# Kernel optimization log

Measured on AMD Instinct MI355X. Metric: run time of the kernel, lower is better.

The kernel has to match this reference:

```python
import jax, jax.numpy as jnp
import numpy as np

N_NODES = 100000
N_EDGES = 1600000
D = 128
N_LAYERS = 3
N_GRAPHS = 128


def setup_inputs() -> dict:
    key = jax.random.key(0)
    ks = jax.random.split(key, 8)
    x = jax.random.normal(ks[0], (N_NODES, D), dtype=jnp.float32)
    # stacked GIN-MLP params (all layers are D->D since hidden_dim == in_dim)
    scale = 1.0 / np.sqrt(D)
    W1 = jax.random.normal(ks[1], (N_LAYERS, D, D), dtype=jnp.float32) * scale
    b1 = jax.random.normal(ks[2], (N_LAYERS, D), dtype=jnp.float32) * 0.01
    W2 = jax.random.normal(ks[3], (N_LAYERS, D, D), dtype=jnp.float32) * scale
    b2 = jax.random.normal(ks[4], (N_LAYERS, D), dtype=jnp.float32) * 0.01
    edge_index = jax.random.randint(ks[5], (2, N_EDGES), 0, N_NODES, dtype=jnp.int64)
    batch = jnp.sort(jax.random.randint(ks[6], (N_NODES,), 0, N_GRAPHS, dtype=jnp.int64))
    return {"x": x, "W1": W1, "b1": b1, "W2": W2, "b2": b2,
            "edge_index": edge_index, "batch": batch}


def reference(x, W1, b1, W2, b2, edge_index, batch):
    src = edge_index[0]
    dst = edge_index[1]
    n = x.shape[0]
    eps = jnp.float32(0.0)  # GIN eps (PyG default, not trained)
    for i in range(N_LAYERS):
        # gather neighbor features along edges, scatter-add to destination nodes
        agg = jax.ops.segment_sum(x[src], dst, num_segments=n)  # [N, D]
        h = (1.0 + eps) * x + agg
        h = jax.nn.relu(h @ W1[i] + b1[i])
        x = h @ W2[i] + b2[i]
    # sum-pool readout per graph
    h_G = jax.ops.segment_sum(x, batch, num_segments=N_GRAPHS)  # [G, D]
    return h_G
```

## Files before the change

kernel.cpp:

```cpp
#include <hip/hip_runtime.h>
#include <hip/hip_bf16.h>
#include <stdint.h>

#define N_NODES 100000
#define N_EDGES 1600000
#define DIM 128
#define N_GRAPHS 128
#define LDA 136

#define NBKT 392
#define BCAP 6144
#define BP   5632

#define NBIN_BLK 391
#define CVT_BLK 3125

typedef unsigned int uint32;
typedef unsigned short ushort16;

typedef __bf16 bf16x8 __attribute__((ext_vector_type(8)));
typedef float fx4 __attribute__((ext_vector_type(4)));

__device__ __forceinline__ float bfLo(uint32 u){ return __builtin_bit_cast(float, (uint32)(u << 16)); }
__device__ __forceinline__ float bfHi(uint32 u){ return __builtin_bit_cast(float, (uint32)(u & 0xFFFF0000u)); }
__device__ __forceinline__ ushort16 f2bf(float f){
  uint32 u = __builtin_bit_cast(uint32, f);
  u = u + 0x7FFFu + ((u >> 16) & 1u);
  return (ushort16)(u >> 16);
}
__device__ __forceinline__ uint32 pack2(float a, float b){
  return (uint32)f2bf(a) | ((uint32)f2bf(b) << 16);
}

__global__ __launch_bounds__(512) void k_prep(const float* __restrict__ x,
                                              const float* __restrict__ W1, const float* __restrict__ W2,
                                              const int* __restrict__ ei,
                                              ushort16* __restrict__ P, ushort16* __restrict__ Q,
                                              ushort16* __restrict__ Wf,
                                              int* __restrict__ bucketCursor,
                                              int* __restrict__ temp){
  __shared__ int hist[NBKT];
  __shared__ int base[NBKT];
  __shared__ int gbase[NBKT];
  __shared__ int scanbuf[512];
  __shared__ int sVal[4096];
  __shared__ unsigned short sBkt[4096];

  int bb = blockIdx.x;
  int t  = threadIdx.x;

  if (bb < NBIN_BLK){
    int e0 = bb * 4096;
    for (int i = t; i < NBKT; i += 512) hist[i] = 0;
    __syncthreads();

    int   myv[8];
    short myb[8];
    short myr[8];
    #pragma unroll
    for (int it = 0; it < 8; ++it){
      int e = e0 + it*512 + t;
      int v = 0; short b = -1; short r = 0;
      if (e < N_EDGES){
        int s = ei[e];
        int d = ei[N_EDGES + e];
        b = (short)(d >> 8);
        v = s | ((d & 255) << 17);
        r = (short)atomicAdd(&hist[b], 1);
      }
      myv[it] = v; myb[it] = b; myr[it] = r;
    }
    __syncthreads();

    scanbuf[t] = (t < NBKT) ? hist[t] : 0;
    __syncthreads();
    for (int off = 1; off < 512; off <<= 1){
      int x2 = 0;
      if (t >= off) x2 = scanbuf[t - off];
      __syncthreads();
      scanbuf[t] += x2;
      __syncthreads();
    }
    if (t < NBKT){
      base[t]  = scanbuf[t] - hist[t];
      gbase[t] = atomicAdd(&bucketCursor[t], hist[t]);
    }
    __syncthreads();

    #pragma unroll
    for (int it = 0; it < 8; ++it){
      if (myb[it] >= 0){
        int p = base[myb[it]] + myr[it];
        sVal[p] = myv[it];
        sBkt[p] = (unsigned short)myb[it];
      }
    }
    __syncthreads();

    int cnt = scanbuf[NBKT - 1];
    for (int p = t; p < cnt; p += 512){
      int b = sBkt[p];
      int g = gbase[b] + (p - base[b]);
      if (g < BCAP) temp[b*BCAP + g] = sVal[p];
    }
    return;
  }

  if (bb < NBIN_BLK + CVT_BLK){
    int idx = ((bb - NBIN_BLK)*512 + t) * 8;
    float4 v0 = *(const float4*)(x + idx);
    float4 v1 = *(const float4*)(x + idx + 4);
    uint4 o;
    o.x = pack2(v0.x, v0.y); o.y = pack2(v0.z, v0.w);
    o.z = pack2(v1.x, v1.y); o.w = pack2(v1.z, v1.w);
    *(uint4*)(P + idx) = o;
    return;
  }

  if (bb == NBIN_BLK + CVT_BLK){
    uint4 z = {0u,0u,0u,0u};
    if (t < 16)                *(uint4*)(P + (size_t)N_NODES*128 + t*8)      = z;
    else if (t < 32)           *(uint4*)(Q + (size_t)N_NODES*128 + (t-16)*8) = z;
    return;
  }

  int tid = (bb - (NBIN_BLK + CVT_BLK + 1))*512 + t;
  int layer = tid >> 12;
  int rem   = tid & 4095;
  int mat   = rem >> 11;
  int nt    = (rem >> 8) & 7;
  int kt    = (rem >> 6) & 3;
  int lane  = rem & 63;
  int kg = lane >> 4, m = lane & 15;
  int n  = nt*16 + m;
  int kb = kt*32 + kg*8;
  const float* src = (mat ? W2 : W1) + layer*16384;
  uint4 o;
  o.x = pack2(src[(kb+0)*128 + n], src[(kb+1)*128 + n]);
  o.y = pack2(src[(kb+2)*128 + n], src[(kb+3)*128 + n]);
  o.z = pack2(src[(kb+4)*128 + n], src[(kb+5)*128 + n]);
  o.w = pack2(src[(kb+6)*128 + n], src[(kb+7)*128 + n]);
  *(uint4*)(Wf + ((((size_t)(layer*2+mat)*8 + nt)*4 + kt)*64 + lane)*8) = o;
}

__global__ __launch_bounds__(512) void k_binB(const int* __restrict__ temp,
                                              const int* __restrict__ bucketCursor,
                                              int* __restrict__ rowptr,
                                              int* __restrict__ rowlen,
                                              int* __restrict__ colx){
  __shared__ int counts[256];
  __shared__ int sc[256];
  __shared__ int cur[256];
  __shared__ int stage[BCAP];
  __shared__ int sorted[BCAP];
  int b = blockIdx.x, t = threadIdx.x;
  int cnt = min(bucketCursor[b], BCAP);
  int gb  = b * BP;
  const int* src = temp + b*BCAP;

  if (t < 256) counts[t] = 0;
  __syncthreads();
  for (int p = t; p < cnt; p += 512){
    int v = src[p];
    stage[p] = v;
    atomicAdd(&counts[v >> 17], 1);
  }
  __syncthreads();

  int len = 0, plen = 0;
  if (t < 256){
    len  = counts[t];
    plen = (len + 3) & ~3;
    sc[t] = plen;
  }
  __syncthreads();
  for (int off = 1; off < 256; off <<= 1){
    int x = 0;
    if (t < 256 && t >= off) x = sc[t - off];
    __syncthreads();
    if (t < 256) sc[t] += x;
    __syncthreads();
  }
  int excl = 0;
  if (t < 256){
    excl = sc[t] - plen;
    cur[t] = excl;
    int node = b*256 + t;
    if (node < N_NODES){ rowptr[node] = gb + excl; rowlen[node] = plen; }
  }
  __syncthreads();

  for (int p = t; p < cnt; p += 512){
    int v = stage[p];
    int d = v >> 17;
    int pos = atomicAdd(&cur[d], 1);
    sorted[pos] = v & 0x1FFFF;
  }
  __syncthreads();

  if (t < 256){
    for (int k = len; k < plen; ++k) sorted[excl + k] = N_NODES;
  }
  __syncthreads();

  int total = min(sc[255], BP);
  for (int p = t; p < total; p += 512) colx[gb + p] = sorted[p];
}

template<bool LAST>
__global__ __launch_bounds__(256, 8) void k_gin(const ushort16* __restrict__ xb, ushort16* __restrict__ hb,
                                                const ushort16* __restrict__ Wt1, const float* __restrict__ b1,
                                                const ushort16* __restrict__ Wt2, const float* __restrict__ b2,
                                                const int* __restrict__ rowptr, const int* __restrict__ rowlen,
                                                const int* __restrict__ colx,
                                                const int* __restrict__ batch, float* __restrict__ outp){
  __shared__ __attribute__((aligned(16))) ushort16 sA[32 * LDA];
  __shared__ int sOff[32];
  __shared__ int sLen[32];
  __shared__ int sBat[32];

  int t = threadIdx.x;
  int row0 = blockIdx.x * 32;

  if (t < 32){
    int gg = row0 + t;
    sOff[t] = rowptr[gg];
    sLen[t] = rowlen[gg];
    if (LAST) sBat[t] = batch[gg];
  }
  __syncthreads();

  int wave = t >> 6, lane = t & 63;
  int g = lane >> 4, o = lane & 15;
  const uint32* xw = (const uint32*)xb;

  for (int ni = 0; ni < 8; ++ni){
    int ln  = wave*8 + ni;
    int j   = __builtin_amdgcn_readfirstlane(sOff[ln]);
    int end = j + __builtin_amdgcn_readfirstlane(sLen[ln]);

    float f0=0.f,f1=0.f,f2=0.f,f3=0.f,f4=0.f,f5=0.f,f6=0.f,f7=0.f;

    while (j + 8 <= end){
      int4 c0 = *(const int4*)(colx + j);
      int4 c1 = *(const int4*)(colx + j + 4);
      int r0ab = (g & 1) ? c0.y : c0.x;
      int r0cd = (g & 1) ? c0.w : c0.z;
      int r0   = (g & 2) ? r0cd : r0ab;
      int r1ab = (g & 1) ? c1.y : c1.x;
      int r1cd = (g & 1) ? c1.w : c1.z;
      int r1   = (g & 2) ? r1cd : r1ab;
      uint4 u0 = *(const uint4*)(xw + (size_t)r0*64 + o*4);
      uint4 u1 = *(const uint4*)(xw + (size_t)r1*64 + o*4);
      f0 += bfLo(u0.x); f1 += bfHi(u0.x); f2 += bfLo(u0.y); f3 += bfHi(u0.y);
      f4 += bfLo(u0.z); f5 += bfHi(u0.z); f6 += bfLo(u0.w); f7 += bfHi(u0.w);
      f0 += bfLo(u1.x); f1 += bfHi(u1.x); f2 += bfLo(u1.y); f3 += bfHi(u1.y);
      f4 += bfLo(u1.z); f5 += bfHi(u1.z); f6 += bfLo(u1.w); f7 += bfHi(u1.w);
      j += 8;
    }
    if (j < end){
      int4 c0 = *(const int4*)(colx + j);
      int rab = (g & 1) ? c0.y : c0.x;
      int rcd = (g & 1) ? c0.w : c0.z;
      int r0  = (g & 2) ? rcd : rab;
      uint4 u0 = *(const uint4*)(xw + (size_t)r0*64 + o*4);
      f0 += bfLo(u0.x); f1 += bfHi(u0.x); f2 += bfLo(u0.y); f3 += bfHi(u0.y);
      f4 += bfLo(u0.z); f5 += bfHi(u0.z); f6 += bfLo(u0.w); f7 += bfHi(u0.w);
    }

    f0 += __shfl_xor(f0, 16, 64); f1 += __shfl_xor(f1, 16, 64);
    f2 += __shfl_xor(f2, 16, 64); f3 += __shfl_xor(f3, 16, 64);
    f4 += __shfl_xor(f4, 16, 64); f5 += __shfl_xor(f5, 16, 64);
    f6 += __shfl_xor(f6, 16, 64); f7 += __shfl_xor(f7, 16, 64);
    f0 += __shfl_xor(f0, 32, 64); f1 += __shfl_xor(f1, 32, 64);
    f2 += __shfl_xor(f2, 32, 64); f3 += __shfl_xor(f3, 32, 64);
    f4 += __shfl_xor(f4, 32, 64); f5 += __shfl_xor(f5, 32, 64);
    f6 += __shfl_xor(f6, 32, 64); f7 += __shfl_xor(f7, 32, 64);

    if (g == 0){
      int gn = row0 + ln;
      uint4 xv = *(const uint4*)(xw + (size_t)gn*64 + o*4);
      uint4 r;
      r.x = pack2(f0 + bfLo(xv.x), f1 + bfHi(xv.x));
      r.y = pack2(f2 + bfLo(xv.y), f3 + bfHi(xv.y));
      r.z = pack2(f4 + bfLo(xv.z), f5 + bfHi(xv.z));
      r.w = pack2(f6 + bfLo(xv.w), f7 + bfHi(xv.w));
      *(uint4*)(sA + ln*LDA + o*8) = r;
    }
  }
  __syncthreads();

  int m = lane & 15, kg = lane >> 4;
  int nt0 = wave*2, nt1 = wave*2 + 1;

  fx4 acc[2][2];
  #pragma unroll
  for (int mt = 0; mt < 2; ++mt){ acc[mt][0] = (fx4){0,0,0,0}; acc[mt][1] = (fx4){0,0,0,0}; }

  #pragma unroll
  for (int kt = 0; kt < 4; ++kt){
    bf16x8 ba = *(const bf16x8*)(Wt1 + ((nt0*4 + kt)*64 + lane)*8);
    bf16x8 bb = *(const bf16x8*)(Wt1 + ((nt1*4 + kt)*64 + lane)*8);
    #pragma unroll
    for (int mt = 0; mt < 2; ++mt){
      bf16x8 av = *(const bf16x8*)(sA + (mt*16 + m)*LDA + kg*8 + kt*32);
      acc[mt][0] = __builtin_amdgcn_mfma_f32_16x16x32_bf16(av, ba, acc[mt][0], 0, 0, 0);
      acc[mt][1] = __builtin_amdgcn_mfma_f32_16x16x32_bf16(av, bb, acc[mt][1], 0, 0, 0);
    }
  }
  float bva = b1[nt0*16 + m];
  float bvb = b1[nt1*16 + m];
  __syncthreads();

  #pragma unroll
  for (int mt = 0; mt < 2; ++mt){
    #pragma unroll
    for (int r = 0; r < 4; ++r){
      int row = mt*16 + kg*4 + r;
      sA[row*LDA + nt0*16 + m] = f2bf(fmaxf(acc[mt][0][r] + bva, 0.f));
      sA[row*LDA + nt1*16 + m] = f2bf(fmaxf(acc[mt][1][r] + bvb, 0.f));
    }
  }
  float cva = b2[nt0*16 + m];
  float cvb = b2[nt1*16 + m];
  #pragma unroll
  for (int mt = 0; mt < 2; ++mt){ acc[mt][0] = (fx4){0,0,0,0}; acc[mt][1] = (fx4){0,0,0,0}; }
  __syncthreads();

  #pragma unroll
  for (int kt = 0; kt < 4; ++kt){
    bf16x8 ba = *(const bf16x8*)(Wt2 + ((nt0*4 + kt)*64 + lane)*8);
    bf16x8 bb = *(const bf16x8*)(Wt2 + ((nt1*4 + kt)*64 + lane)*8);
    #pragma unroll
    for (int mt = 0; mt < 2; ++mt){
      bf16x8 av = *(const bf16x8*)(sA + (mt*16 + m)*LDA + kg*8 + kt*32);
      acc[mt][0] = __builtin_amdgcn_mfma_f32_16x16x32_bf16(av, ba, acc[mt][0], 0, 0, 0);
      acc[mt][1] = __builtin_amdgcn_mfma_f32_16x16x32_bf16(av, bb, acc[mt][1], 0, 0, 0);
    }
  }

  if constexpr (!LAST){
    #pragma unroll
    for (int mt = 0; mt < 2; ++mt){
      #pragma unroll
      for (int r = 0; r < 4; ++r){
        int row = row0 + mt*16 + kg*4 + r;
        hb[row*128 + nt0*16 + m] = f2bf(acc[mt][0][r] + cva);
        hb[row*128 + nt1*16 + m] = f2bf(acc[mt][1][r] + cvb);
      }
    }
  } else {
    float sum0 = 0.f, sum1 = 0.f; int curg = -1;
    #pragma unroll
    for (int mt = 0; mt < 2; ++mt){
      #pragma unroll
      for (int r = 0; r < 4; ++r){
        int lrow = mt*16 + kg*4 + r;
        int gg = sBat[lrow];
        if (gg != curg){
          if (curg >= 0){
            atomicAdd(&outp[curg*128 + nt0*16 + m], sum0);
            atomicAdd(&outp[curg*128 + nt1*16 + m], sum1);
          }
          curg = gg; sum0 = 0.f; sum1 = 0.f;
        }
        sum0 += acc[mt][0][r] + cva;
        sum1 += acc[mt][1][r] + cvb;
      }
    }
    if (curg >= 0){
      atomicAdd(&outp[curg*128 + nt0*16 + m], sum0);
      atomicAdd(&outp[curg*128 + nt1*16 + m], sum1);
    }
  }
}

extern "C" void kernel_launch(void* const* d_in, const int* in_sizes, int n_in,
                              void* d_out, int out_size, void* d_ws, size_t ws_size,
                              hipStream_t stream) {
  const float* x   = (const float*)d_in[0];
  const float* W1  = (const float*)d_in[1];
  const float* b1  = (const float*)d_in[2];
  const float* W2  = (const float*)d_in[3];
  const float* b2  = (const float*)d_in[4];
  const int*   ei  = (const int*)d_in[5];
  const int*   bat = (const int*)d_in[6];
  float* out = (float*)d_out;

  char* w = (char*)d_ws;
  auto carve = [&](size_t bytes) -> char* {
    char* p = w; w += (bytes + 255) & ~(size_t)255; return p;
  };
  ushort16* P    = (ushort16*)carve((size_t)(N_NODES+1) * DIM * 2);
  ushort16* Q    = (ushort16*)carve((size_t)(N_NODES+1) * DIM * 2);
  ushort16* Wf   = (ushort16*)carve((size_t)3 * 2 * 16384 * 2);
  int* rowptr    = (int*)carve((size_t)N_NODES * 4);
  int* rowlen    = (int*)carve((size_t)N_NODES * 4);
  int* colx      = (int*)carve((size_t)NBKT * BP * 4);
  int* bucketCursor = (int*)carve((NBKT + 1) * 4);
  int* temp      = (int*)Q;

  hipMemsetAsync(bucketCursor, 0, (NBKT + 1) * 4, stream);
  hipMemsetAsync(d_out, 0, (size_t)N_GRAPHS * DIM * 4, stream);

  k_prep<<<NBIN_BLK + CVT_BLK + 1 + 24, 512, 0, stream>>>(x, W1, W2, ei, P, Q, Wf,
                                                          bucketCursor, temp);
  k_binB<<<NBKT, 512, 0, stream>>>(temp, bucketCursor, rowptr, rowlen, colx);

  const int ginGrid = N_NODES / 32;

  k_gin<false><<<ginGrid, 256, 0, stream>>>(P, Q, Wf + 0*16384, b1 + 0*128, Wf + 1*16384, b2 + 0*128,
                                            rowptr, rowlen, colx, bat, out);
  k_gin<false><<<ginGrid, 256, 0, stream>>>(Q, P, Wf + 2*16384, b1 + 1*128, Wf + 3*16384, b2 + 1*128,
                                            rowptr, rowlen, colx, bat, out);
  k_gin<true><<<ginGrid, 256, 0, stream>>>(P, Q, Wf + 4*16384, b1 + 2*128, Wf + 5*16384, b2 + 2*128,
                                           rowptr, rowlen, colx, bat, out);
}
```

Baseline: 344.2 us.

## Process 64 nodes per GIN block and gather one node per 16-lane group

Doubles the rows per block from 32 to 64 so each wave's MLP weight fragments are reused across four M-tiles. The aggregation loop is restructured so each 16-lane group owns a whole node and issues eight independent row gathers per step, with no cross-lane shuffle reduction. The aim is more memory-level parallelism in the gather and less repeated weight loading per row. In exchange, lanes in a wave now take divergent loop counts when node degrees differ, register use rises with occupancy lowered to 6, and bounds checks are added for the partial last block.

```diff
diff --git a/kernel.cpp b/kernel.cpp
--- a/kernel.cpp
+++ b/kernel.cpp
@@ -208,101 +208,94 @@
 }
 
 template<bool LAST>
-__global__ __launch_bounds__(256, 8) void k_gin(const ushort16* __restrict__ xb, ushort16* __restrict__ hb,
+__global__ __launch_bounds__(256, 6) void k_gin(const ushort16* __restrict__ xb, ushort16* __restrict__ hb,
                                                 const ushort16* __restrict__ Wt1, const float* __restrict__ b1,
                                                 const ushort16* __restrict__ Wt2, const float* __restrict__ b2,
                                                 const int* __restrict__ rowptr, const int* __restrict__ rowlen,
                                                 const int* __restrict__ colx,
                                                 const int* __restrict__ batch, float* __restrict__ outp){
-  __shared__ __attribute__((aligned(16))) ushort16 sA[32 * LDA];
-  __shared__ int sOff[32];
-  __shared__ int sLen[32];
-  __shared__ int sBat[32];
+  __shared__ __attribute__((aligned(16))) ushort16 sA[64 * LDA];
+  __shared__ int sOff[64];
+  __shared__ int sLen[64];
+  __shared__ int sBat[64];
 
   int t = threadIdx.x;
-  int row0 = blockIdx.x * 32;
-
-  if (t < 32){
+  int row0 = blockIdx.x * 64;
+
+  if (t < 64){
     int gg = row0 + t;
-    sOff[t] = rowptr[gg];
-    sLen[t] = rowlen[gg];
-    if (LAST) sBat[t] = batch[gg];
+    int off = 0, len = 0, bg = 0;
+    if (gg < N_NODES){
+      off = rowptr[gg]; len = rowlen[gg];
+      if (LAST) bg = batch[gg];
+    }
+    sOff[t] = off; sLen[t] = len; sBat[t] = bg;
   }
   __syncthreads();
 
   int wave = t >> 6, lane = t & 63;
-  int g = lane >> 4, o = lane & 15;
+  int g16 = lane >> 4, o = lane & 15;
   const uint32* xw = (const uint32*)xb;
 
-  for (int ni = 0; ni < 8; ++ni){
-    int ln  = wave*8 + ni;
-    int j   = __builtin_amdgcn_readfirstlane(sOff[ln]);
-    int end = j + __builtin_amdgcn_readfirstlane(sLen[ln]);
-
-    float f0=0.f,f1=0.f,f2=0.f,f3=0.f,f4=0.f,f5=0.f,f6=0.f,f7=0.f;
-
-    while (j + 8 <= end){
-      int4 c0 = *(const int4*)(colx + j);
-      int4 c1 = *(const int4*)(colx + j + 4);
-      int r0ab = (g & 1) ? c0.y : c0.x;
-      int r0cd = (g & 1) ? c0.w : c0.z;
-      int r0   = (g & 2) ? r0cd : r0ab;
-      int r1ab = (g & 1) ? c1.y : c1.x;
-      int r1cd = (g & 1) ? c1.w : c1.z;
-      int r1   = (g & 2) ? r1cd : r1ab;
-      uint4 u0 = *(const uint4*)(xw + (size_t)r0*64 + o*4);
-      uint4 u1 = *(const uint4*)(xw + (size_t)r1*64 + o*4);
-      f0 += bfLo(u0.x); f1 += bfHi(u0.x); f2 += bfLo(u0.y); f3 += bfHi(u0.y);
-      f4 += bfLo(u0.z); f5 += bfHi(u0.z); f6 += bfLo(u0.w); f7 += bfHi(u0.w);
-      f0 += bfLo(u1.x); f1 += bfHi(u1.x); f2 += bfLo(u1.y); f3 += bfHi(u1.y);
-      f4 += bfLo(u1.z); f5 += bfHi(u1.z); f6 += bfLo(u1.w); f7 += bfHi(u1.w);
-      j += 8;
-    }
-    if (j < end){
-      int4 c0 = *(const int4*)(colx + j);
-      int rab = (g & 1) ? c0.y : c0.x;
-      int rcd = (g & 1) ? c0.w : c0.z;
-      int r0  = (g & 2) ? rcd : rab;
-      uint4 u0 = *(const uint4*)(xw + (size_t)r0*64 + o*4);
-      f0 += bfLo(u0.x); f1 += bfHi(u0.x); f2 += bfLo(u0.y); f3 += bfHi(u0.y);
-      f4 += bfLo(u0.z); f5 += bfHi(u0.z); f6 += bfLo(u0.w); f7 += bfHi(u0.w);
-    }
-
-    f0 += __shfl_xor(f0, 16, 64); f1 += __shfl_xor(f1, 16, 64);
-    f2 += __shfl_xor(f2, 16, 64); f3 += __shfl_xor(f3, 16, 64);
-    f4 += __shfl_xor(f4, 16, 64); f5 += __shfl_xor(f5, 16, 64);
-    f6 += __shfl_xor(f6, 16, 64); f7 += __shfl_xor(f7, 16, 64);
-    f0 += __shfl_xor(f0, 32, 64); f1 += __shfl_xor(f1, 32, 64);
-    f2 += __shfl_xor(f2, 32, 64); f3 += __shfl_xor(f3, 32, 64);
-    f4 += __shfl_xor(f4, 32, 64); f5 += __shfl_xor(f5, 32, 64);
-    f6 += __shfl_xor(f6, 32, 64); f7 += __shfl_xor(f7, 32, 64);
-
-    if (g == 0){
-      int gn = row0 + ln;
-      uint4 xv = *(const uint4*)(xw + (size_t)gn*64 + o*4);
-      uint4 r;
-      r.x = pack2(f0 + bfLo(xv.x), f1 + bfHi(xv.x));
-      r.y = pack2(f2 + bfLo(xv.y), f3 + bfHi(xv.y));
-      r.z = pack2(f4 + bfLo(xv.z), f5 + bfHi(xv.z));
-      r.w = pack2(f6 + bfLo(xv.w), f7 + bfHi(xv.w));
-      *(uint4*)(sA + ln*LDA + o*8) = r;
-    }
-  }
+#define GATH(r) (*(const uint4*)(xw + (size_t)(r)*64 + o*4))
+#define ACC8(u) do { \
+    a0 += (fx4){ bfLo((u).x), bfHi((u).x), bfLo((u).y), bfHi((u).y) }; \
+    a1 += (fx4){ bfLo((u).z), bfHi((u).z), bfLo((u).w), bfHi((u).w) }; \
+  } while(0)
+
+  #pragma unroll
+  for (int q = 0; q < 4; ++q){
+    int ln  = wave*16 + q*4 + g16;
+    int j   = sOff[ln];
+    int len = sLen[ln];
+    int gn  = row0 + ln;
+    fx4 a0 = (fx4){0.f,0.f,0.f,0.f};
+    fx4 a1 = (fx4){0.f,0.f,0.f,0.f};
+
+    int rd = 0;
+    for (; rd + 8 <= len; rd += 8){
+      int4 c0 = *(const int4*)(colx + j + rd);
+      int4 c1 = *(const int4*)(colx + j + rd + 4);
+      uint4 u0 = GATH(c0.x); uint4 u1 = GATH(c0.y);
+      uint4 u2 = GATH(c0.z); uint4 u3 = GATH(c0.w);
+      uint4 u4 = GATH(c1.x); uint4 u5 = GATH(c1.y);
+      uint4 u6 = GATH(c1.z); uint4 u7 = GATH(c1.w);
+      ACC8(u0); ACC8(u1); ACC8(u2); ACC8(u3);
+      ACC8(u4); ACC8(u5); ACC8(u6); ACC8(u7);
+    }
+    if (rd < len){
+      int4 c0 = *(const int4*)(colx + j + rd);
+      uint4 u0 = GATH(c0.x); uint4 u1 = GATH(c0.y);
+      uint4 u2 = GATH(c0.z); uint4 u3 = GATH(c0.w);
+      ACC8(u0); ACC8(u1); ACC8(u2); ACC8(u3);
+    }
+
+    uint4 xv = {0u,0u,0u,0u};
+    if (gn < N_NODES) xv = *(const uint4*)(xw + (size_t)gn*64 + o*4);
+    uint4 r;
+    r.x = pack2(a0[0]+bfLo(xv.x), a0[1]+bfHi(xv.x));
+    r.y = pack2(a0[2]+bfLo(xv.y), a0[3]+bfHi(xv.y));
+    r.z = pack2(a1[0]+bfLo(xv.z), a1[1]+bfHi(xv.z));
+    r.w = pack2(a1[2]+bfLo(xv.w), a1[3]+bfHi(xv.w));
+    *(uint4*)(sA + ln*LDA + o*8) = r;
+  }
+#undef GATH
+#undef ACC8
   __syncthreads();
 
   int m = lane & 15, kg = lane >> 4;
   int nt0 = wave*2, nt1 = wave*2 + 1;
 
-  fx4 acc[2][2];
-  #pragma unroll
-  for (int mt = 0; mt < 2; ++mt){ acc[mt][0] = (fx4){0,0,0,0}; acc[mt][1] = (fx4){0,0,0,0}; }
+  fx4 acc[4][2];
+  #pragma unroll
+  for (int mt = 0; mt < 4; ++mt){ acc[mt][0] = (fx4){0,0,0,0}; acc[mt][1] = (fx4){0,0,0,0}; }
 
   #pragma unroll
   for (int kt = 0; kt < 4; ++kt){
     bf16x8 ba = *(const bf16x8*)(Wt1 + ((nt0*4 + kt)*64 + lane)*8);
     bf16x8 bb = *(const bf16x8*)(Wt1 + ((nt1*4 + kt)*64 + lane)*8);
     #pragma unroll
-    for (int mt = 0; mt < 2; ++mt){
+    for (int mt = 0; mt < 4; ++mt){
       bf16x8 av = *(const bf16x8*)(sA + (mt*16 + m)*LDA + kg*8 + kt*32);
       acc[mt][0] = __builtin_amdgcn_mfma_f32_16x16x32_bf16(av, ba, acc[mt][0], 0, 0, 0);
       acc[mt][1] = __builtin_amdgcn_mfma_f32_16x16x32_bf16(av, bb, acc[mt][1], 0, 0, 0);
@@ -313,7 +306,7 @@
   __syncthreads();
 
   #pragma unroll
-  for (int mt = 0; mt < 2; ++mt){
+  for (int mt = 0; mt < 4; ++mt){
     #pragma unroll
     for (int r = 0; r < 4; ++r){
       int row = mt*16 + kg*4 + r;
@@ -324,7 +317,7 @@
   float cva = b2[nt0*16 + m];
   float cvb = b2[nt1*16 + m];
   #pragma unroll
-  for (int mt = 0; mt < 2; ++mt){ acc[mt][0] = (fx4){0,0,0,0}; acc[mt][1] = (fx4){0,0,0,0}; }
+  for (int mt = 0; mt < 4; ++mt){ acc[mt][0] = (fx4){0,0,0,0}; acc[mt][1] = (fx4){0,0,0,0}; }
   __syncthreads();
 
   #pragma unroll
@@ -332,7 +325,7 @@
     bf16x8 ba = *(const bf16x8*)(Wt2 + ((nt0*4 + kt)*64 + lane)*8);
     bf16x8 bb = *(const bf16x8*)(Wt2 + ((nt1*4 + kt)*64 + lane)*8);
     #pragma unroll
-    for (int mt = 0; mt < 2; ++mt){
+    for (int mt = 0; mt < 4; ++mt){
       bf16x8 av = *(const bf16x8*)(sA + (mt*16 + m)*LDA + kg*8 + kt*32);
       acc[mt][0] = __builtin_amdgcn_mfma_f32_16x16x32_bf16(av, ba, acc[mt][0], 0, 0, 0);
       acc[mt][1] = __builtin_amdgcn_mfma_f32_16x16x32_bf16(av, bb, acc[mt][1], 0, 0, 0);
@@ -341,31 +334,36 @@
 
   if constexpr (!LAST){
     #pragma unroll
-    for (int mt = 0; mt < 2; ++mt){
+    for (int mt = 0; mt < 4; ++mt){
       #pragma unroll
       for (int r = 0; r < 4; ++r){
         int row = row0 + mt*16 + kg*4 + r;
-        hb[row*128 + nt0*16 + m] = f2bf(acc[mt][0][r] + cva);
-        hb[row*128 + nt1*16 + m] = f2bf(acc[mt][1][r] + cvb);
+        if (row < N_NODES){
+          hb[row*128 + nt0*16 + m] = f2bf(acc[mt][0][r] + cva);
+          hb[row*128 + nt1*16 + m] = f2bf(acc[mt][1][r] + cvb);
+        }
       }
     }
   } else {
     float sum0 = 0.f, sum1 = 0.f; int curg = -1;
     #pragma unroll
-    for (int mt = 0; mt < 2; ++mt){
+    for (int mt = 0; mt < 4; ++mt){
       #pragma unroll
       for (int r = 0; r < 4; ++r){
         int lrow = mt*16 + kg*4 + r;
-        int gg = sBat[lrow];
-        if (gg != curg){
-          if (curg >= 0){
-            atomicAdd(&outp[curg*128 + nt0*16 + m], sum0);
-            atomicAdd(&outp[curg*128 + nt1*16 + m], sum1);
+        int grow = row0 + lrow;
+        if (grow < N_NODES){
+          int gg = sBat[lrow];
+          if (gg != curg){
+            if (curg >= 0){
+              atomicAdd(&outp[curg*128 + nt0*16 + m], sum0);
+              atomicAdd(&outp[curg*128 + nt1*16 + m], sum1);
+            }
+            curg = gg; sum0 = 0.f; sum1 = 0.f;
           }
-          curg = gg; sum0 = 0.f; sum1 = 0.f;
+          sum0 += acc[mt][0][r] + cva;
+          sum1 += acc[mt][1][r] + cvb;
         }
-        sum0 += acc[mt][0][r] + cva;
-        sum1 += acc[mt][1][r] + cvb;
       }
     }
     if (curg >= 0){
@@ -407,7 +405,7 @@
                                                           bucketCursor, temp);
   k_binB<<<NBKT, 512, 0, stream>>>(temp, bucketCursor, rowptr, rowlen, colx);
 
-  const int ginGrid = N_NODES / 32;
+  const int ginGrid = (N_NODES + 63) / 64;
 
   k_gin<false><<<ginGrid, 256, 0, stream>>>(P, Q, Wf + 0*16384, b1 + 0*128, Wf + 1*16384, b2 + 0*128,
                                             rowptr, rowlen, colx, bat, out);
```

New measurement: 331.0 us. -3.8%, faster.
